# Kernel optimization log

Hardware: AMD Instinct MI355X
Metric: run time of the kernel (lower is better)

The kernel has to match this reference:

```python
import math
import jax, jax.numpy as jnp
import numpy as np

B, Q, K, D = 32, 1024, 1024, 128
MASK_VALUE = -1000000.0


def setup_inputs() -> dict:
    key = jax.random.key(0)
    kq, kk, kv, kl = jax.random.split(key, 4)
    return {
        "queries": jax.random.normal(kq, (B, Q, D), dtype=jnp.float32),
        "keys": jax.random.normal(kk, (B, K, D), dtype=jnp.float32),
        "values": jax.random.normal(kv, (B, K, D), dtype=jnp.float32),
        "valid_lens": jax.random.randint(kl, (B,), 1, K + 1, dtype=jnp.int32),
    }


def reference(queries, keys, values, valid_lens):
    d = queries.shape[-1]
    # scores: [B, Q, K]
    scores = jnp.einsum("bqd,bkd->bqk", queries, keys) / math.sqrt(d)
    # key-padding mask: position k valid iff k < valid_lens[b] (broadcast over queries)
    mask = jnp.arange(keys.shape[1])[None, None, :] < valid_lens[:, None, None]
    scores = jnp.where(mask, scores, MASK_VALUE)
    attn = jax.nn.softmax(scores, axis=-1)
    # dropout p=0.0 -> identity
    return jnp.einsum("bqk,bkv->bqv", attn, values)
```

## Files before the change

### kernel.cpp

```cpp
#include <hip/hip_runtime.h>
#include <math.h>

typedef _Float16 f16;
typedef __attribute__((ext_vector_type(8))) _Float16 f16x8;
typedef __attribute__((ext_vector_type(4))) _Float16 f16x4;
typedef __attribute__((ext_vector_type(4))) float f32x4;

constexpr int BATCH = 32;
constexpr int QL = 1024;
constexpr int KL = 1024;
constexpr int D = 128;
constexpr int BQ = 64;
constexpr int BK = 64;
constexpr int DKP = 136;
constexpr int BKP = 72;

#define CSC 0.12752863187087177f

static __device__ __forceinline__ f16x4 pk4(float x, float y, float z, float w) {
  auto a = __builtin_amdgcn_cvt_pkrtz(x, y);
  auto b = __builtin_amdgcn_cvt_pkrtz(z, w);
  f16x4 h;
  h[0] = (f16)a[0]; h[1] = (f16)a[1]; h[2] = (f16)b[0]; h[3] = (f16)b[1];
  return h;
}
static __device__ __forceinline__ f16x8 pk8(float4 u, float4 v) {
  f16x4 a = pk4(u.x, u.y, u.z, u.w);
  f16x4 b = pk4(v.x, v.y, v.z, v.w);
  f16x8 h;
  h[0] = a[0]; h[1] = a[1]; h[2] = a[2]; h[3] = a[3];
  h[4] = b[0]; h[5] = b[1]; h[6] = b[2]; h[7] = b[3];
  return h;
}

template <int CTRL>
static __device__ __forceinline__ float dppf(float v) {
  int x = __float_as_int(v);
  x = __builtin_amdgcn_update_dpp(x, x, CTRL, 0xf, 0xf, false);
  return __int_as_float(x);
}
static __device__ __forceinline__ float rmax16(float v) {
  v = fmaxf(v, dppf<0xB1>(v));
  v = fmaxf(v, dppf<0x4E>(v));
  v = fmaxf(v, dppf<0x141>(v));
  v = fmaxf(v, dppf<0x140>(v));
  return v;
}
static __device__ __forceinline__ float rsum16(float v) {
  v += dppf<0xB1>(v);
  v += dppf<0x4E>(v);
  v += dppf<0x141>(v);
  v += dppf<0x140>(v);
  return v;
}

__global__ __launch_bounds__(256, 2)
void attn_fwd(const float* __restrict__ Qp, const float* __restrict__ Kp,
              const float* __restrict__ Vp, const int* __restrict__ VLp,
              float* __restrict__ Op) {
  __shared__ f16 sK[2][BK][DKP];
  __shared__ f16 sVT[2][D][BKP];
  __shared__ f16 sP[4][16][BKP];
  __shared__ int sN[32];
  __shared__ int sB;

  const int tid  = threadIdx.x;
  const int wave = tid >> 6, lane = tid & 63;
  const int l16  = lane & 15, quad = lane >> 4;

  if (tid < 32) sN[tid] = (VLp[tid] + BK - 1) / BK;
  __syncthreads();
  if (tid < 32) {
    int nb = sN[tid], r = 0;
    #pragma unroll
    for (int k = 0; k < 32; ++k) {
      int nk = sN[k];
      r += (nk > nb) || (nk == nb && k < tid);
    }
    sN[tid] = r;
  }
  __syncthreads();
  const int c = blockIdx.x & 255;
  const int s = (blockIdx.x < 256) ? c : (511 - c);
  if (tid < 32 && sN[tid] == (s >> 4)) sB = tid;
  __syncthreads();
  const int b  = sB;
  const int qt = s & 15;
  const int vl = VLp[b];

  const float* Kb = Kp + (size_t)b * KL * D;
  const float* Vb = Vp + (size_t)b * KL * D;
  const int ntiles = (vl + BK - 1) / BK;

  float4 kreg[8], vreg[8];

  {
    const float4* Kt = (const float4*)Kb;
    #pragma unroll
    for (int i = 0; i < 4; ++i) {
      int cc = tid + i * 256;
      int row = cc >> 4, d04 = (cc & 15) * 2;
      kreg[2 * i]     = Kt[row * 32 + d04];
      kreg[2 * i + 1] = Kt[row * 32 + d04 + 1];
    }
    #pragma unroll
    for (int i = 0; i < 2; ++i) {
      int f = tid + i * 256;
      const float* base = Vb + (size_t)((f & 15) * 4) * D + (f >> 4) * 4;
      vreg[i * 4 + 0] = *(const float4*)(base);
      vreg[i * 4 + 1] = *(const float4*)(base + D);
      vreg[i * 4 + 2] = *(const float4*)(base + 2 * D);
      vreg[i * 4 + 3] = *(const float4*)(base + 3 * D);
    }
  }

  const float* Qb = Qp + ((size_t)(b * QL + qt * BQ + wave * 16 + l16)) * D;
  f16x8 qfrag[4];
  #pragma unroll
  for (int kc = 0; kc < 4; ++kc) {
    const float* p = Qb + kc * 32 + quad * 8;
    qfrag[kc] = pk8(*(const float4*)p, *(const float4*)(p + 4));
  }

  float m2[4]   = {-INFINITY, -INFINITY, -INFINITY, -INFINITY};
  float lsum[4] = {0.f, 0.f, 0.f, 0.f};
  f32x4 o[8];
  #pragma unroll
  for (int dt = 0; dt < 8; ++dt) o[dt] = (f32x4){0.f, 0.f, 0.f, 0.f};

  #pragma unroll
  for (int i = 0; i < 4; ++i) {
    int cc = tid + i * 256;
    int row = cc >> 4, d0 = (cc & 15) * 8;
    int rp = (row & 3) * 16 + (row >> 2);
    *(f16x8*)&sK[0][rp][d0] = pk8(kreg[2 * i], kreg[2 * i + 1]);
  }
  #pragma unroll
  for (int i = 0; i < 2; ++i) {
    int f = tid + i * 256;
    int k0 = (f & 15) * 4, d0 = (f >> 4) * 4;
    float4 r0 = vreg[i*4+0], r1 = vreg[i*4+1], r2 = vreg[i*4+2], r3 = vreg[i*4+3];
    *(f16x4*)&sVT[0][d0 + 0][k0] = pk4(r0.x, r1.x, r2.x, r3.x);
    *(f16x4*)&sVT[0][d0 + 1][k0] = pk4(r0.y, r1.y, r2.y, r3.y);
    *(f16x4*)&sVT[0][d0 + 2][k0] = pk4(r0.z, r1.z, r2.z, r3.z);
    *(f16x4*)&sVT[0][d0 + 3][k0] = pk4(r0.w, r1.w, r2.w, r3.w);
  }
  __syncthreads();

  for (int t = 0; t < ntiles; ++t) {
    const int cur = t & 1, nxt = cur ^ 1;
    const bool more = (t + 1 < ntiles);

    if (more) {
      const float4* Kt = (const float4*)(Kb + (size_t)(t + 1) * BK * D);
      #pragma unroll
      for (int i = 0; i < 4; ++i) {
        int cc = tid + i * 256;
        int row = cc >> 4, d04 = (cc & 15) * 2;
        kreg[2 * i]     = Kt[row * 32 + d04];
        kreg[2 * i + 1] = Kt[row * 32 + d04 + 1];
      }
      const float* Vt = Vb + (size_t)(t + 1) * BK * D;
      #pragma unroll
      for (int i = 0; i < 2; ++i) {
        int f = tid + i * 256;
        const float* base = Vt + (size_t)((f & 15) * 4) * D + (f >> 4) * 4;
        vreg[i * 4 + 0] = *(const float4*)(base);
        vreg[i * 4 + 1] = *(const float4*)(base + D);
        vreg[i * 4 + 2] = *(const float4*)(base + 2 * D);
        vreg[i * 4 + 3] = *(const float4*)(base + 3 * D);
      }
    }

    f32x4 sv[4];
    #pragma unroll
    for (int ct = 0; ct < 4; ++ct) {
      f32x4 cacc = (f32x4){0.f, 0.f, 0.f, 0.f};
      #pragma unroll
      for (int kc = 0; kc < 4; ++kc) {
        f16x8 kf = *(const f16x8*)&sK[cur][ct * 16 + l16][kc * 32 + quad * 8];
        cacc = __builtin_amdgcn_mfma_f32_16x16x32_f16(qfrag[kc], kf, cacc, 0, 0, 0);
      }
      sv[ct] = cacc;
    }

    #pragma unroll
    for (int ct = 0; ct < 4; ++ct) {
      bool ok = (t * BK + l16 * 4 + ct) < vl;
      #pragma unroll
      for (int r = 0; r < 4; ++r)
        sv[ct][r] = ok ? sv[ct][r] * CSC : -1.0e9f;
    }

    float mnew[4], alpha[4];
    #pragma unroll
    for (int r = 0; r < 4; ++r) {
      float v = fmaxf(fmaxf(sv[0][r], sv[1][r]), fmaxf(sv[2][r], sv[3][r]));
      v = rmax16(v);
      mnew[r]  = fmaxf(m2[r], v);
      alpha[r] = __builtin_amdgcn_exp2f(m2[r] - mnew[r]);
      m2[r]    = mnew[r];
    }
    #pragma unroll
    for (int r = 0; r < 4; ++r) {
      float ls = 0.f;
      #pragma unroll
      for (int ct = 0; ct < 4; ++ct) {
        float p = __builtin_amdgcn_exp2f(sv[ct][r] - mnew[r]);
        sv[ct][r] = p;
        ls += p;
      }
      lsum[r] = lsum[r] * alpha[r] + rsum16(ls);
      *(f16x4*)&sP[wave][quad * 4 + r][l16 * 4] =
          pk4(sv[0][r], sv[1][r], sv[2][r], sv[3][r]);
      #pragma unroll
      for (int dt = 0; dt < 8; ++dt) o[dt][r] *= alpha[r];
    }

    asm volatile("s_waitcnt lgkmcnt(0)" ::: "memory");

    #pragma unroll
    for (int ks = 0; ks < 2; ++ks) {
      f16x8 pf = *(const f16x8*)&sP[wave][l16][ks * 32 + quad * 8];
      #pragma unroll
      for (int dt = 0; dt < 8; ++dt) {
        f16x8 vf = *(const f16x8*)&sVT[cur][dt * 16 + l16][ks * 32 + quad * 8];
        o[dt] = __builtin_amdgcn_mfma_f32_16x16x32_f16(pf, vf, o[dt], 0, 0, 0);
      }
    }

    if (more) {
      #pragma unroll
      for (int i = 0; i < 4; ++i) {
        int cc = tid + i * 256;
        int row = cc >> 4, d0 = (cc & 15) * 8;
        int rp = (row & 3) * 16 + (row >> 2);
        *(f16x8*)&sK[nxt][rp][d0] = pk8(kreg[2 * i], kreg[2 * i + 1]);
      }
      #pragma unroll
      for (int i = 0; i < 2; ++i) {
        int f = tid + i * 256;
        int k0 = (f & 15) * 4, d0 = (f >> 4) * 4;
        float4 r0 = vreg[i*4+0], r1 = vreg[i*4+1], r2 = vreg[i*4+2], r3 = vreg[i*4+3];
        *(f16x4*)&sVT[nxt][d0 + 0][k0] = pk4(r0.x, r1.x, r2.x, r3.x);
        *(f16x4*)&sVT[nxt][d0 + 1][k0] = pk4(r0.y, r1.y, r2.y, r3.y);
        *(f16x4*)&sVT[nxt][d0 + 2][k0] = pk4(r0.z, r1.z, r2.z, r3.z);
        *(f16x4*)&sVT[nxt][d0 + 3][k0] = pk4(r0.w, r1.w, r2.w, r3.w);
      }
    }
    __syncthreads();
  }

  float* Ob = Op + ((size_t)(b * QL + qt * BQ + wave * 16)) * D;
  #pragma unroll
  for (int r = 0; r < 4; ++r) {
    float inv = 1.0f / lsum[r];
    int row = quad * 4 + r;
    #pragma unroll
    for (int dt = 0; dt < 8; ++dt)
      Ob[(size_t)row * D + dt * 16 + l16] = o[dt][r] * inv;
  }
}

extern "C" void kernel_launch(void* const* d_in, const int* in_sizes, int n_in,
                              void* d_out, int out_size, void* d_ws, size_t ws_size,
                              hipStream_t stream) {
  const float* Qp = (const float*)d_in[0];
  const float* Kp = (const float*)d_in[1];
  const float* Vp = (const float*)d_in[2];
  const int*   VL = (const int*)d_in[3];
  float* Op = (float*)d_out;

  attn_fwd<<<dim3(QL / BQ * BATCH), dim3(256), 0, stream>>>(Qp, Kp, Vp, VL, Op);
}
```

Before: 119.2 us.

## Prefetch K/V two tiles ahead and remap blocks to XCDs by batch

Register prefetching now runs two tiles ahead. Two register sets (kA/vA, kB/vB) alternate in a manually unrolled loop, so each global load has about two compute phases to complete. The per-tile __syncthreads is replaced by an explicit lgkmcnt wait plus s_barrier. Block-to-batch mapping is rewritten so each XCD (blockIdx & 7) gets a balanced mix of long and short batches and the blocks of one batch share an XCD, for L2 reuse of K/V. This doubles prefetch register usage, which risks spills or lower occupancy under launch_bounds(256,2).

Measured after the change: 127.9 us. 1.07x slower.

```diff
diff --git a/kernel.cpp b/kernel.cpp
--- a/kernel.cpp
+++ b/kernel.cpp
@@ -54,6 +54,115 @@
   return v;
 }
 
+#define ISSUE(KR, VR, T)                                                   \
+  do {                                                                     \
+    const float4* Kt = (const float4*)(Kb + (size_t)(T) * BK * D);         \
+    _Pragma("unroll")                                                      \
+    for (int i_ = 0; i_ < 4; ++i_) {                                       \
+      int cc_ = tid + i_ * 256;                                            \
+      int row_ = cc_ >> 4, d04_ = (cc_ & 15) * 2;                          \
+      KR[2 * i_]     = Kt[row_ * 32 + d04_];                               \
+      KR[2 * i_ + 1] = Kt[row_ * 32 + d04_ + 1];                           \
+    }                                                                      \
+    const float* Vt = Vb + (size_t)(T) * BK * D;                           \
+    _Pragma("unroll")                                                      \
+    for (int i_ = 0; i_ < 2; ++i_) {                                       \
+      int f_ = tid + i_ * 256;                                             \
+      const float* base_ = Vt + (size_t)((f_ & 15) * 4) * D + (f_ >> 4) * 4; \
+      VR[i_ * 4 + 0] = *(const float4*)(base_);                            \
+      VR[i_ * 4 + 1] = *(const float4*)(base_ + D);                        \
+      VR[i_ * 4 + 2] = *(const float4*)(base_ + 2 * D);                    \
+      VR[i_ * 4 + 3] = *(const float4*)(base_ + 3 * D);                    \
+    }                                                                      \
+  } while (0)
+
+#define DRAIN(KR, VR, NB)                                                  \
+  do {                                                                     \
+    _Pragma("unroll")                                                      \
+    for (int i_ = 0; i_ < 4; ++i_) {                                       \
+      int cc_ = tid + i_ * 256;                                            \
+      int row_ = cc_ >> 4, d0_ = (cc_ & 15) * 8;                           \
+      int rp_ = (row_ & 3) * 16 + (row_ >> 2);                             \
+      *(f16x8*)&sK[NB][rp_][d0_] = pk8(KR[2 * i_], KR[2 * i_ + 1]);        \
+    }                                                                      \
+    _Pragma("unroll")                                                      \
+    for (int i_ = 0; i_ < 2; ++i_) {                                       \
+      int f_ = tid + i_ * 256;                                             \
+      int k0_ = (f_ & 15) * 4, d0_ = (f_ >> 4) * 4;                        \
+      float4 r0_ = VR[i_*4+0], r1_ = VR[i_*4+1], r2_ = VR[i_*4+2], r3_ = VR[i_*4+3]; \
+      *(f16x4*)&sVT[NB][d0_ + 0][k0_] = pk4(r0_.x, r1_.x, r2_.x, r3_.x);   \
+      *(f16x4*)&sVT[NB][d0_ + 1][k0_] = pk4(r0_.y, r1_.y, r2_.y, r3_.y);   \
+      *(f16x4*)&sVT[NB][d0_ + 2][k0_] = pk4(r0_.z, r1_.z, r2_.z, r3_.z);   \
+      *(f16x4*)&sVT[NB][d0_ + 3][k0_] = pk4(r0_.w, r1_.w, r2_.w, r3_.w);   \
+    }                                                                      \
+  } while (0)
+
+#define TILE_BARRIER()                                                     \
+  do {                                                                     \
+    asm volatile("s_waitcnt lgkmcnt(0)" ::: "memory");                     \
+    __builtin_amdgcn_s_barrier();                                          \
+    asm volatile("" ::: "memory");                                         \
+  } while (0)
+
+#define COMPUTE(CB)                                                        \
+  do {                                                                     \
+    f32x4 sv[4];                                                           \
+    _Pragma("unroll")                                                      \
+    for (int ct = 0; ct < 4; ++ct) {                                       \
+      f32x4 cacc = (f32x4){0.f, 0.f, 0.f, 0.f};                            \
+      _Pragma("unroll")                                                    \
+      for (int kc = 0; kc < 4; ++kc) {                                     \
+        f16x8 kf = *(const f16x8*)&sK[CB][ct * 16 + l16][kc * 32 + quad * 8]; \
+        cacc = __builtin_amdgcn_mfma_f32_16x16x32_f16(qfrag[kc], kf, cacc, 0, 0, 0); \
+      }                                                                    \
+      sv[ct] = cacc;                                                       \
+    }                                                                      \
+     \
+    _Pragma("unroll")                                                      \
+    for (int ct = 0; ct < 4; ++ct) {                                       \
+      bool ok = (t * BK + l16 * 4 + ct) < vl;                              \
+      _Pragma("unroll")                                                    \
+      for (int r = 0; r < 4; ++r)                                          \
+        sv[ct][r] = ok ? sv[ct][r] * CSC : -1.0e9f;                        \
+    }                                                                      \
+                  \
+    float mnew[4], alpha[4];                                               \
+    _Pragma("unroll")                                                      \
+    for (int r = 0; r < 4; ++r) {                                          \
+      float v = fmaxf(fmaxf(sv[0][r], sv[1][r]), fmaxf(sv[2][r], sv[3][r])); \
+      v = rmax16(v);                                                       \
+      mnew[r]  = fmaxf(m2[r], v);                                          \
+      alpha[r] = __builtin_amdgcn_exp2f(m2[r] - mnew[r]);                  \
+      m2[r]    = mnew[r];                                                  \
+    }                                                                      \
+    _Pragma("unroll")                                                      \
+    for (int r = 0; r < 4; ++r) {                                          \
+      float ls = 0.f;                                                      \
+      _Pragma("unroll")                                                    \
+      for (int ct = 0; ct < 4; ++ct) {                                     \
+        float p = __builtin_amdgcn_exp2f(sv[ct][r] - mnew[r]);             \
+        sv[ct][r] = p;                                                     \
+        ls += p;                                                           \
+      }                                                                    \
+      lsum[r] = lsum[r] * alpha[r] + rsum16(ls);                           \
+      *(f16x4*)&sP[wave][quad * 4 + r][l16 * 4] =                          \
+          pk4(sv[0][r], sv[1][r], sv[2][r], sv[3][r]);                     \
+      _Pragma("unroll")                                                    \
+      for (int dt = 0; dt < 8; ++dt) o[dt][r] *= alpha[r];                 \
+    }                                                                      \
+           \
+    asm volatile("s_waitcnt lgkmcnt(0)" ::: "memory");                     \
+    _Pragma("unroll")                                                      \
+    for (int ks = 0; ks < 2; ++ks) {                                       \
+      f16x8 pf = *(const f16x8*)&sP[wave][l16][ks * 32 + quad * 8];        \
+      _Pragma("unroll")                                                    \
+      for (int dt = 0; dt < 8; ++dt) {                                     \
+        f16x8 vf = *(const f16x8*)&sVT[CB][dt * 16 + l16][ks * 32 + quad * 8]; \
+        o[dt] = __builtin_amdgcn_mfma_f32_16x16x32_f16(pf, vf, o[dt], 0, 0, 0); \
+      }                                                                    \
+    }                                                                      \
+  } while (0)
+
 __global__ __launch_bounds__(256, 2)
 void attn_fwd(const float* __restrict__ Qp, const float* __restrict__ Kp,
               const float* __restrict__ Vp, const int* __restrict__ VLp,
@@ -62,7 +171,7 @@
   __shared__ f16 sVT[2][D][BKP];
   __shared__ f16 sP[4][16][BKP];
   __shared__ int sN[32];
-  __shared__ int sB;
+  __shared__ int sI[32];
 
   const int tid  = threadIdx.x;
   const int wave = tid >> 6, lane = tid & 63;
@@ -77,50 +186,40 @@
       int nk = sN[k];
       r += (nk > nb) || (nk == nb && k < tid);
     }
-    sN[tid] = r;
+    sI[r] = tid;
   }
   __syncthreads();
-  const int c = blockIdx.x & 255;
-  const int s = (blockIdx.x < 256) ? c : (511 - c);
-  if (tid < 32 && sN[tid] == (s >> 4)) sB = tid;
-  __syncthreads();
-  const int b  = sB;
-  const int qt = s & 15;
+  const int xcd = blockIdx.x & 7;
+  const int j   = (int)blockIdx.x >> 3;
+  const int jj  = (j < 32) ? j : (95 - j);
+  const int lr  = jj >> 4;
+  const int qt  = jj & 15;
+  const int grank = (lr == 0) ? xcd : (lr == 1) ? (15 - xcd)
+                  : (lr == 2) ? (16 + xcd) : (31 - xcd);
+  const int b  = sI[grank];
   const int vl = VLp[b];
 
   const float* Kb = Kp + (size_t)b * KL * D;
   const float* Vb = Vp + (size_t)b * KL * D;
   const int ntiles = (vl + BK - 1) / BK;
 
-  float4 kreg[8], vreg[8];
-
-  {
-    const float4* Kt = (const float4*)Kb;
-    #pragma unroll
-    for (int i = 0; i < 4; ++i) {
-      int cc = tid + i * 256;
-      int row = cc >> 4, d04 = (cc & 15) * 2;
-      kreg[2 * i]     = Kt[row * 32 + d04];
-      kreg[2 * i + 1] = Kt[row * 32 + d04 + 1];
-    }
-    #pragma unroll
-    for (int i = 0; i < 2; ++i) {
-      int f = tid + i * 256;
-      const float* base = Vb + (size_t)((f & 15) * 4) * D + (f >> 4) * 4;
-      vreg[i * 4 + 0] = *(const float4*)(base);
-      vreg[i * 4 + 1] = *(const float4*)(base + D);
-      vreg[i * 4 + 2] = *(const float4*)(base + 2 * D);
-      vreg[i * 4 + 3] = *(const float4*)(base + 3 * D);
-    }
-  }
+  float4 kA[8], vA[8], kB[8], vB[8];
 
   const float* Qb = Qp + ((size_t)(b * QL + qt * BQ + wave * 16 + l16)) * D;
-  f16x8 qfrag[4];
+  float4 qtmp[8];
   #pragma unroll
   for (int kc = 0; kc < 4; ++kc) {
     const float* p = Qb + kc * 32 + quad * 8;
-    qfrag[kc] = pk8(*(const float4*)p, *(const float4*)(p + 4));
-  }
+    qtmp[2 * kc]     = *(const float4*)p;
+    qtmp[2 * kc + 1] = *(const float4*)(p + 4);
+  }
+
+  ISSUE(kA, vA, 0);
+  if (ntiles > 1) ISSUE(kB, vB, 1);
+
+  f16x8 qfrag[4];
+  #pragma unroll
+  for (int kc = 0; kc < 4; ++kc) qfrag[kc] = pk8(qtmp[2 * kc], qtmp[2 * kc + 1]);
 
   float m2[4]   = {-INFINITY, -INFINITY, -INFINITY, -INFINITY};
   float lsum[4] = {0.f, 0.f, 0.f, 0.f};
@@ -128,127 +227,23 @@
   #pragma unroll
   for (int dt = 0; dt < 8; ++dt) o[dt] = (f32x4){0.f, 0.f, 0.f, 0.f};
 
-  #pragma unroll
-  for (int i = 0; i < 4; ++i) {
-    int cc = tid + i * 256;
-    int row = cc >> 4, d0 = (cc & 15) * 8;
-    int rp = (row & 3) * 16 + (row >> 2);
-    *(f16x8*)&sK[0][rp][d0] = pk8(kreg[2 * i], kreg[2 * i + 1]);
-  }
-  #pragma unroll
-  for (int i = 0; i < 2; ++i) {
-    int f = tid + i * 256;
-    int k0 = (f & 15) * 4, d0 = (f >> 4) * 4;
-    float4 r0 = vreg[i*4+0], r1 = vreg[i*4+1], r2 = vreg[i*4+2], r3 = vreg[i*4+3];
-    *(f16x4*)&sVT[0][d0 + 0][k0] = pk4(r0.x, r1.x, r2.x, r3.x);
-    *(f16x4*)&sVT[0][d0 + 1][k0] = pk4(r0.y, r1.y, r2.y, r3.y);
-    *(f16x4*)&sVT[0][d0 + 2][k0] = pk4(r0.z, r1.z, r2.z, r3.z);
-    *(f16x4*)&sVT[0][d0 + 3][k0] = pk4(r0.w, r1.w, r2.w, r3.w);
-  }
-  __syncthreads();
-
-  for (int t = 0; t < ntiles; ++t) {
-    const int cur = t & 1, nxt = cur ^ 1;
-    const bool more = (t + 1 < ntiles);
-
-    if (more) {
-      const float4* Kt = (const float4*)(Kb + (size_t)(t + 1) * BK * D);
-      #pragma unroll
-      for (int i = 0; i < 4; ++i) {
-        int cc = tid + i * 256;
-        int row = cc >> 4, d04 = (cc & 15) * 2;
-        kreg[2 * i]     = Kt[row * 32 + d04];
-        kreg[2 * i + 1] = Kt[row * 32 + d04 + 1];
-      }
-      const float* Vt = Vb + (size_t)(t + 1) * BK * D;
-      #pragma unroll
-      for (int i = 0; i < 2; ++i) {
-        int f = tid + i * 256;
-        const float* base = Vt + (size_t)((f & 15) * 4) * D + (f >> 4) * 4;
-        vreg[i * 4 + 0] = *(const float4*)(base);
-        vreg[i * 4 + 1] = *(const float4*)(base + D);
-        vreg[i * 4 + 2] = *(const float4*)(base + 2 * D);
-        vreg[i * 4 + 3] = *(const float4*)(base + 3 * D);
-      }
-    }
-
-    f32x4 sv[4];
-    #pragma unroll
-    for (int ct = 0; ct < 4; ++ct) {
-      f32x4 cacc = (f32x4){0.f, 0.f, 0.f, 0.f};
-      #pragma unroll
-      for (int kc = 0; kc < 4; ++kc) {
-        f16x8 kf = *(const f16x8*)&sK[cur][ct * 16 + l16][kc * 32 + quad * 8];
-        cacc = __builtin_amdgcn_mfma_f32_16x16x32_f16(qfrag[kc], kf, cacc, 0, 0, 0);
-      }
-      sv[ct] = cacc;
-    }
-
-    #pragma unroll
-    for (int ct = 0; ct < 4; ++ct) {
-      bool ok = (t * BK + l16 * 4 + ct) < vl;
-      #pragma unroll
-      for (int r = 0; r < 4; ++r)
-        sv[ct][r] = ok ? sv[ct][r] * CSC : -1.0e9f;
-    }
-
-    float mnew[4], alpha[4];
-    #pragma unroll
-    for (int r = 0; r < 4; ++r) {
-      float v = fmaxf(fmaxf(sv[0][r], sv[1][r]), fmaxf(sv[2][r], sv[3][r]));
-      v = rmax16(v);
-      mnew[r]  = fmaxf(m2[r], v);
-      alpha[r] = __builtin_amdgcn_exp2f(m2[r] - mnew[r]);
-      m2[r]    = mnew[r];
-    }
-    #pragma unroll
-    for (int r = 0; r < 4; ++r) {
-      float ls = 0.f;
-      #pragma unroll
-      for (int ct = 0; ct < 4; ++ct) {
-        float p = __builtin_amdgcn_exp2f(sv[ct][r] - mnew[r]);
-        sv[ct][r] = p;
-        ls += p;
-      }
-      lsum[r] = lsum[r] * alpha[r] + rsum16(ls);
-      *(f16x4*)&sP[wave][quad * 4 + r][l16 * 4] =
-          pk4(sv[0][r], sv[1][r], sv[2][r], sv[3][r]);
-      #pragma unroll
-      for (int dt = 0; dt < 8; ++dt) o[dt][r] *= alpha[r];
-    }
-
-    asm volatile("s_waitcnt lgkmcnt(0)" ::: "memory");
-
-    #pragma unroll
-    for (int ks = 0; ks < 2; ++ks) {
-      f16x8 pf = *(const f16x8*)&sP[wave][l16][ks * 32 + quad * 8];
-      #pragma unroll
-      for (int dt = 0; dt < 8; ++dt) {
-        f16x8 vf = *(const f16x8*)&sVT[cur][dt * 16 + l16][ks * 32 + quad * 8];
-        o[dt] = __builtin_amdgcn_mfma_f32_16x16x32_f16(pf, vf, o[dt], 0, 0, 0);
-      }
-    }
-
-    if (more) {
-      #pragma unroll
-      for (int i = 0; i < 4; ++i) {
-        int cc = tid + i * 256;
-        int row = cc >> 4, d0 = (cc & 15) * 8;
-        int rp = (row & 3) * 16 + (row >> 2);
-        *(f16x8*)&sK[nxt][rp][d0] = pk8(kreg[2 * i], kreg[2 * i + 1]);
-      }
-      #pragma unroll
-      for (int i = 0; i < 2; ++i) {
-        int f = tid + i * 256;
-        int k0 = (f & 15) * 4, d0 = (f >> 4) * 4;
-        float4 r0 = vreg[i*4+0], r1 = vreg[i*4+1], r2 = vreg[i*4+2], r3 = vreg[i*4+3];
-        *(f16x4*)&sVT[nxt][d0 + 0][k0] = pk4(r0.x, r1.x, r2.x, r3.x);
-        *(f16x4*)&sVT[nxt][d0 + 1][k0] = pk4(r0.y, r1.y, r2.y, r3.y);
-        *(f16x4*)&sVT[nxt][d0 + 2][k0] = pk4(r0.z, r1.z, r2.z, r3.z);
-        *(f16x4*)&sVT[nxt][d0 + 3][k0] = pk4(r0.w, r1.w, r2.w, r3.w);
-      }
-    }
-    __syncthreads();
+  DRAIN(kA, vA, 0);
+  TILE_BARRIER();
+
+  int t = 0;
+  for (;;) {
+    if (t + 2 < ntiles) ISSUE(kA, vA, t + 2);
+    COMPUTE(0);
+    if (t + 1 >= ntiles) break;
+    DRAIN(kB, vB, 1);
+    TILE_BARRIER();
+    ++t;
+    if (t + 2 < ntiles) ISSUE(kB, vB, t + 2);
+    COMPUTE(1);
+    if (t + 1 >= ntiles) break;
+    DRAIN(kA, vA, 0);
+    TILE_BARRIER();
+    ++t;
   }
 
   float* Ob = Op + ((size_t)(b * QL + qt * BQ + wave * 16)) * D;
```

## Map batches to XCDs for L2 reuse, hoist Q loads, lighten barriers

Applied to the files above, without the earlier changes.

Work is now assigned so that every workgroup sharing a batch's K/V runs on the same XCD. The mapping uses blockIdx mod 8 as the XCD, and batches are spread in a snake order by length rank. This is meant to improve L2 hit rates for K/V, which are re-read by 16 query tiles. It also replaces a barrier by building an inverse rank table, so one __syncthreads is dropped. Q global loads are issued before the K/V prologue loads to overlap latency, and __syncthreads is replaced by an explicit lgkmcnt wait plus s_barrier, with the risk that ordering of outstanding vector memory ops is relaxed.

Result: faster. 116.3 us (-2.5%).

```diff
diff --git a/kernel.cpp b/kernel.cpp
--- a/kernel.cpp
+++ b/kernel.cpp
@@ -62,7 +62,7 @@
   __shared__ f16 sVT[2][D][BKP];
   __shared__ f16 sP[4][16][BKP];
   __shared__ int sN[32];
-  __shared__ int sB;
+  __shared__ int sI[32];
 
   const int tid  = threadIdx.x;
   const int wave = tid >> 6, lane = tid & 63;
@@ -77,15 +77,17 @@
       int nk = sN[k];
       r += (nk > nb) || (nk == nb && k < tid);
     }
-    sN[tid] = r;
+    sI[r] = tid;
   }
   __syncthreads();
-  const int c = blockIdx.x & 255;
-  const int s = (blockIdx.x < 256) ? c : (511 - c);
-  if (tid < 32 && sN[tid] == (s >> 4)) sB = tid;
-  __syncthreads();
-  const int b  = sB;
-  const int qt = s & 15;
+  const int xcd = blockIdx.x & 7;
+  const int j   = (int)blockIdx.x >> 3;
+  const int jj  = (j < 32) ? j : (95 - j);
+  const int lr  = jj >> 4;
+  const int qt  = jj & 15;
+  const int grank = (lr == 0) ? xcd : (lr == 1) ? (15 - xcd)
+                  : (lr == 2) ? (16 + xcd) : (31 - xcd);
+  const int b  = sI[grank];
   const int vl = VLp[b];
 
   const float* Kb = Kp + (size_t)b * KL * D;
@@ -93,6 +95,15 @@
   const int ntiles = (vl + BK - 1) / BK;
 
   float4 kreg[8], vreg[8];
+
+  const float* Qb = Qp + ((size_t)(b * QL + qt * BQ + wave * 16 + l16)) * D;
+  float4 qtmp[8];
+  #pragma unroll
+  for (int kc = 0; kc < 4; ++kc) {
+    const float* p = Qb + kc * 32 + quad * 8;
+    qtmp[2 * kc]     = *(const float4*)p;
+    qtmp[2 * kc + 1] = *(const float4*)(p + 4);
+  }
 
   {
     const float4* Kt = (const float4*)Kb;
@@ -114,13 +125,9 @@
     }
   }
 
-  const float* Qb = Qp + ((size_t)(b * QL + qt * BQ + wave * 16 + l16)) * D;
   f16x8 qfrag[4];
   #pragma unroll
-  for (int kc = 0; kc < 4; ++kc) {
-    const float* p = Qb + kc * 32 + quad * 8;
-    qfrag[kc] = pk8(*(const float4*)p, *(const float4*)(p + 4));
-  }
+  for (int kc = 0; kc < 4; ++kc) qfrag[kc] = pk8(qtmp[2 * kc], qtmp[2 * kc + 1]);
 
   float m2[4]   = {-INFINITY, -INFINITY, -INFINITY, -INFINITY};
   float lsum[4] = {0.f, 0.f, 0.f, 0.f};
@@ -145,7 +152,9 @@
     *(f16x4*)&sVT[0][d0 + 2][k0] = pk4(r0.z, r1.z, r2.z, r3.z);
     *(f16x4*)&sVT[0][d0 + 3][k0] = pk4(r0.w, r1.w, r2.w, r3.w);
   }
-  __syncthreads();
+  asm volatile("s_waitcnt lgkmcnt(0)" ::: "memory");
+  __builtin_amdgcn_s_barrier();
+  asm volatile("" ::: "memory");
 
   for (int t = 0; t < ntiles; ++t) {
     const int cur = t & 1, nxt = cur ^ 1;
@@ -248,7 +257,9 @@
         *(f16x4*)&sVT[nxt][d0 + 3][k0] = pk4(r0.w, r1.w, r2.w, r3.w);
       }
     }
-    __syncthreads();
+    asm volatile("s_waitcnt lgkmcnt(0)" ::: "memory");
+    __builtin_amdgcn_s_barrier();
+    asm volatile("" ::: "memory");
   }
 
   float* Ob = Op + ((size_t)(b * QL + qt * BQ + wave * 16)) * D;
```
